# Optimization experiments

Hardware: AMD Instinct MI355X
Metric: run time of the kernel (lower is better)

## Reference

```python
import jax, jax.numpy as jnp
import numpy as np
from jax import lax

DIM = 48
HEADS = 8
B, H, W = 4, 256, 256
EPS = 1e-12  # torch F.normalize eps


def conv1x1(x, w):
    # x: [b,c,h,w], w: [out,c] (1x1 conv, no bias)
    return jnp.einsum('bchw,oc->bohw', x, w)


def dwconv3x3(x, w):
    # depthwise 3x3, padding 1; w: [C,1,3,3]
    return lax.conv_general_dilated(
        x, w, window_strides=(1, 1), padding=((1, 1), (1, 1)),
        dimension_numbers=('NCHW', 'OIHW', 'NCHW'),
        feature_group_count=x.shape[1])


def setup_inputs() -> dict:
    key = jax.random.key(0)
    ks = jax.random.split(key, 8)
    s = 0.05
    return {
        'fea_0': jax.random.normal(ks[0], (B, DIM, H, W), jnp.float32),
        'fea_1': jax.random.normal(ks[1], (B, DIM, H, W), jnp.float32),
        'qk_w': jax.random.normal(ks[2], (2 * DIM, DIM), jnp.float32) * s,
        'qk_dw_w': jax.random.normal(ks[3], (2 * DIM, 1, 3, 3), jnp.float32) * s,
        'v_w': jax.random.normal(ks[4], (DIM, DIM), jnp.float32) * s,
        'v_dw_w': jax.random.normal(ks[5], (DIM, 1, 3, 3), jnp.float32) * s,
        'proj_w': jax.random.normal(ks[6], (DIM, DIM), jnp.float32) * s,
        'temperature': jnp.ones((HEADS, 1, 1), jnp.float32),
    }


def reference(fea_0, fea_1, qk_w, qk_dw_w, v_w, v_dw_w, proj_w, temperature):
    b, c, h, w = fea_0.shape
    ch = c // HEADS  # channels per head
    qk = dwconv3x3(conv1x1(fea_0, qk_w), qk_dw_w)
    q, k = jnp.split(qk, 2, axis=1)
    v = dwconv3x3(conv1x1(fea_1, v_w), v_dw_w)
    # [b, head, c_per_head, h*w]
    q = q.reshape(b, HEADS, ch, h * w)
    k = k.reshape(b, HEADS, ch, h * w)
    v = v.reshape(b, HEADS, ch, h * w)
    q = q / jnp.maximum(jnp.linalg.norm(q, axis=-1, keepdims=True), EPS)
    k = k / jnp.maximum(jnp.linalg.norm(k, axis=-1, keepdims=True), EPS)
    attn = jnp.einsum('bhcn,bhdn->bhcd', q, k) * temperature[None]
    attn = jax.nn.softmax(attn, axis=-1)
    out = jnp.einsum('bhcd,bhdn->bhcn', attn, v)
    out = out.reshape(b, c, h, w)
    return conv1x1(out, proj_w)
```

## Files before the change

### kernel.cpp

```cpp
#include <hip/hip_runtime.h>
#include <cstddef>

#define IMG 256
#define HW 65536
#define NB 4
#define NHEADS 8
#define TW 32
#define TH 16
#define HAW 34
#define HAH 18
#define HP2 (HAW*HAH)
#define NTILE 128
#define XSP 24

typedef short bf16x8 __attribute__((ext_vector_type(8)));
typedef float f32x4 __attribute__((ext_vector_type(4)));
typedef float f32x16 __attribute__((ext_vector_type(16)));

__device__ __forceinline__ unsigned short f2bf(float f) {
    unsigned int x = __float_as_uint(f);
    unsigned int r = (x + 0x7fffu + ((x >> 16) & 1u)) >> 16;
    return (unsigned short)r;
}

__device__ __forceinline__ int xcd_map(int bid, int nwg) {
    const int q = nwg >> 3, r = nwg & 7;
    const int x = bid & 7, i = bid >> 3;
    return (x < r ? x * (q + 1) : r * (q + 1) + (x - r) * q) + i;
}

__global__ __launch_bounds__(256) void prep_qcw_kernel(
    const float* __restrict__ qk_w, const float* __restrict__ qk_dw,
    unsigned short* __restrict__ qcwb) {
    const int idx = blockIdx.x * 256 + threadIdx.x;
    const int e16 = idx & 15;
    const int slot = (idx >> 4) & 127;
    const int tk = idx >> 11;
    const int ks = tk % 3;
    const int head = slot >> 4, sub = slot & 15;
    float v = 0.f;
    if (sub < 12) {
        const int row = (sub < 6) ? (head * 6 + sub) : (48 + head * 6 + (sub - 6));
        v = qk_dw[row * 9 + tk / 3] * qk_w[row * 48 + ks * 16 + e16];
    }
    qcwb[idx] = f2bf(v);
}

__global__ __launch_bounds__(512, 2) void fused_qk_stats_kernel(
    const float* __restrict__ fea0, const unsigned short* __restrict__ qcwb,
    float* __restrict__ stats) {
    __shared__ __align__(16) unsigned short xs[HP2][XSP];
    __shared__ __align__(16) unsigned short sg[8][16][72];
    __shared__ float sacc[384];

    const int tid = threadIdx.x;
    const int b = blockIdx.y;
    const int tile = xcd_map(blockIdx.x, NTILE);
    const int tx = tile & 7, ty = tile >> 3;
    const float* fb = fea0 + (size_t)b * 48 * HW;

    for (int i = tid; i < 384; i += 512) sacc[i] = 0.f;

    const int wave = tid >> 6, lane = tid & 63;
    const int l31 = lane & 31, lhi = lane >> 5;
    const int p = wave >> 2, g = wave & 3;

    f32x16 C[2][4];
#pragma unroll
    for (int m = 0; m < 2; ++m)
#pragma unroll
        for (int nf = 0; nf < 4; ++nf)
#pragma unroll
            for (int r = 0; r < 16; ++r) C[m][nf][r] = 0.f;

#pragma unroll
    for (int ks = 0; ks < 3; ++ks) {
        __syncthreads();
        for (int hp = tid; hp < HP2; hp += 512) {
            const int hx = hp % HAW, hy = hp / HAW;
            const int gx = tx * TW + hx - 1, gy = ty * TH + hy - 1;
            const bool inb = ((unsigned)gx < (unsigned)IMG) && ((unsigned)gy < (unsigned)IMG);
            const int pix = inb ? (gy * IMG + gx) : 0;
            bf16x8 t0, t1;
#pragma unroll
            for (int c = 0; c < 8; ++c) {
                t0[c] = (short)f2bf(inb ? fb[(size_t)(ks * 16 + c) * HW + pix] : 0.f);
                t1[c] = (short)f2bf(inb ? fb[(size_t)(ks * 16 + 8 + c) * HW + pix] : 0.f);
            }
            *(bf16x8*)&xs[hp][0] = t0;
            *(bf16x8*)&xs[hp][8] = t1;
        }
        __syncthreads();

#pragma unroll
        for (int tap = 0; tap < 9; ++tap) {
            const int dy = tap / 3, dx = tap % 3;
            const bf16x8 a0 = *(const bf16x8*)&qcwb[(size_t)((tap * 3 + ks) * 128 + p * 64 + l31) * 16 + lhi * 8];
            const bf16x8 a1 = *(const bf16x8*)&qcwb[(size_t)((tap * 3 + ks) * 128 + p * 64 + 32 + l31) * 16 + lhi * 8];
#pragma unroll
            for (int nf = 0; nf < 4; ++nf) {
                const int hrow = (4 * g + nf + dy) * HAW + l31 + dx;
                const bf16x8 bb = *(const bf16x8*)&xs[hrow][lhi * 8];
                C[0][nf] = __builtin_amdgcn_mfma_f32_32x32x16_bf16(a0, bb, C[0][nf], 0, 0, 0);
                C[1][nf] = __builtin_amdgcn_mfma_f32_32x32x16_bf16(a1, bb, C[1][nf], 0, 0, 0);
            }
        }
    }

    const int fr = lane & 15, fg = lane >> 4;

#define DO_STATS(CA, CB, hbase)                                                   \
    {                                                                             \
        _Pragma("unroll")                                                         \
        for (int hh = 0; hh < 2; ++hh) {                                          \
            _Pragma("unroll")                                                     \
            for (int rq = 0; rq < 2; ++rq) {                                      \
                if (!(rq && lhi)) {                                               \
                    _Pragma("unroll")                                             \
                    for (int j = 0; j < 4; ++j) {                                 \
                        const int sub = j + 8 * rq + 4 * lhi;                     \
                        sg[wave][sub][l31] = f2bf(CA[hh * 8 + rq * 4 + j]);       \
                        sg[wave][sub][32 + l31] = f2bf(CB[hh * 8 + rq * 4 + j]);  \
                    }                                                             \
                }                                                                 \
            }                                                                     \
            asm volatile("s_waitcnt lgkmcnt(0)" ::: "memory");                    \
            __builtin_amdgcn_sched_barrier(0);                                    \
            const bf16x8 a0 = *(const bf16x8*)&sg[wave][fr][fg * 8];              \
            const bf16x8 a1 = *(const bf16x8*)&sg[wave][fr][32 + fg * 8];         \
            asm volatile("s_waitcnt lgkmcnt(0)" ::: "memory");                    \
            __builtin_amdgcn_sched_barrier(0);                                    \
            f32x4 c4 = {0.f, 0.f, 0.f, 0.f};                                      \
            c4 = __builtin_amdgcn_mfma_f32_16x16x32_bf16(a0, a0, c4, 0, 0, 0);    \
            c4 = __builtin_amdgcn_mfma_f32_16x16x32_bf16(a1, a1, c4, 0, 0, 0);    \
            const int h = (hbase) + hh;                                           \
            _Pragma("unroll")                                                     \
            for (int r = 0; r < 4; ++r) {                                         \
                const int crow = fg * 4 + r;                                      \
                const float vv = c4[r];                                           \
                if (crow < 6) {                                                   \
                    if (fr == crow) atomicAdd(&sacc[h * 6 + crow], vv);           \
                    else if (fr >= 6 && fr < 12)                                  \
                        atomicAdd(&sacc[96 + h * 36 + crow * 6 + (fr - 6)], vv);  \
                } else if (crow < 12 && fr == crow) {                             \
                    atomicAdd(&sacc[48 + h * 6 + (crow - 6)], vv);                \
                }                                                                 \
            }                                                                     \
        }                                                                         \
    }

#pragma unroll
    for (int m = 0; m < 2; ++m) {
        DO_STATS(C[m][0], C[m][1], p * 4 + m * 2)
        DO_STATS(C[m][2], C[m][3], p * 4 + m * 2)
    }
#undef DO_STATS

    __syncthreads();
    for (int i = tid; i < 384; i += 512) atomicAdd(&stats[b * 384 + i], sacc[i]);
}

__global__ __launch_bounds__(256) void softmax_w2_cw_kernel(
    const float* __restrict__ stats, const float* __restrict__ proj_w,
    const float* __restrict__ temperature, const float* __restrict__ v_w,
    const float* __restrict__ v_dw, unsigned short* __restrict__ cwb) {
    const int b = blockIdx.x;
    const int tid = threadIdx.x;
    __shared__ float attn[NHEADS * 36];
    __shared__ float W2s[48 * 48];
    const float* sb = stats + b * 384;

    if (tid < 48) {
        const int h = tid / 6, cc = tid % 6;
        float nq = fmaxf(sqrtf(sb[tid]), 1e-12f);
        const float tmp = temperature[h];
        float lo[6];
#pragma unroll
        for (int d = 0; d < 6; ++d) {
            const float nk = fmaxf(sqrtf(sb[48 + h * 6 + d]), 1e-12f);
            lo[d] = sb[96 + h * 36 + cc * 6 + d] / (nq * nk) * tmp;
        }
        float m = lo[0];
#pragma unroll
        for (int d = 1; d < 6; ++d) m = fmaxf(m, lo[d]);
        float s = 0.f;
#pragma unroll
        for (int d = 0; d < 6; ++d) { lo[d] = expf(lo[d] - m); s += lo[d]; }
        const float inv = 1.f / s;
#pragma unroll
        for (int d = 0; d < 6; ++d) attn[h * 36 + cc * 6 + d] = lo[d] * inv;
    }
    __syncthreads();

    for (int idx = tid; idx < 48 * 48; idx += 256) {
        const int c = idx / 48, dg = idx % 48;
        const int h = dg / 6, hd = dg % 6;
        float s = 0.f;
#pragma unroll
        for (int cc = 0; cc < 6; ++cc)
            s = fmaf(proj_w[c * 48 + h * 6 + cc], attn[h * 36 + cc * 6 + hd], s);
        W2s[idx] = s;
    }
    __syncthreads();

    unsigned short* cb = cwb + (size_t)b * 27648;
    for (int pp = 0; pp < 9; ++pp) {
        const int pair = pp * 256 + tid;
        const int c = pair / 48, e = pair % 48;
        float acc[9];
#pragma unroll
        for (int t = 0; t < 9; ++t) acc[t] = 0.f;
        for (int d = 0; d < 48; ++d) {
            const float wv = W2s[c * 48 + d] * v_w[d * 48 + e];
#pragma unroll
            for (int t = 0; t < 9; ++t)
                acc[t] = fmaf(wv, v_dw[d * 9 + t], acc[t]);
        }
#pragma unroll
        for (int t = 0; t < 9; ++t)
            cb[(size_t)((t * 3 + (e >> 4)) * 64 + c) * 16 + (e & 15)] = f2bf(acc[t]);
    }
    for (int i = tid; i < 6912; i += 256) {
        const int e16 = i & 15;
        const int cp = 48 + ((i >> 4) & 15);
        const int tk = i >> 8;
        cb[(size_t)(tk * 64 + cp) * 16 + e16] = 0;
    }
}

__global__ __launch_bounds__(512, 2) void conv3x3_out_kernel(
    const float* __restrict__ fea1, const unsigned short* __restrict__ cwb,
    float* __restrict__ out) {
    __shared__ __align__(16) unsigned short xs[HP2][XSP];

    const int tid = threadIdx.x;
    const int b = blockIdx.y;
    const int tile = xcd_map(blockIdx.x, NTILE);
    const int tx = tile & 7, ty = tile >> 3;
    const float* fb = fea1 + (size_t)b * 48 * HW;
    const unsigned short* cb = cwb + (size_t)b * 27648;

    const int wave = tid >> 6, lane = tid & 63;
    const int l31 = lane & 31, lhi = lane >> 5;
    const int m = wave & 1, g = wave >> 1;

    f32x16 C[4];
#pragma unroll
    for (int nf = 0; nf < 4; ++nf)
#pragma unroll
        for (int r = 0; r < 16; ++r) C[nf][r] = 0.f;

#pragma unroll
    for (int ks = 0; ks < 3; ++ks) {
        __syncthreads();
        for (int hp = tid; hp < HP2; hp += 512) {
            const int hx = hp % HAW, hy = hp / HAW;
            const int gx = tx * TW + hx - 1, gy = ty * TH + hy - 1;
            const bool inb = ((unsigned)gx < (unsigned)IMG) && ((unsigned)gy < (unsigned)IMG);
            const int pix = inb ? (gy * IMG + gx) : 0;
            bf16x8 t0, t1;
#pragma unroll
            for (int c = 0; c < 8; ++c) {
                t0[c] = (short)f2bf(inb ? fb[(size_t)(ks * 16 + c) * HW + pix] : 0.f);
                t1[c] = (short)f2bf(inb ? fb[(size_t)(ks * 16 + 8 + c) * HW + pix] : 0.f);
            }
            *(bf16x8*)&xs[hp][0] = t0;
            *(bf16x8*)&xs[hp][8] = t1;
        }
        __syncthreads();

#pragma unroll
        for (int tap = 0; tap < 9; ++tap) {
            const int dy = tap / 3, dx = tap % 3;
            const bf16x8 a = *(const bf16x8*)&cb[(size_t)((tap * 3 + ks) * 64 + m * 32 + l31) * 16 + lhi * 8];
#pragma unroll
            for (int nf = 0; nf < 4; ++nf) {
                const int hrow = (4 * g + nf + dy) * HAW + l31 + dx;
                const bf16x8 bb = *(const bf16x8*)&xs[hrow][lhi * 8];
                C[nf] = __builtin_amdgcn_mfma_f32_32x32x16_bf16(a, bb, C[nf], 0, 0, 0);
            }
        }
    }

    float* ob = out + (size_t)b * 48 * HW;
#pragma unroll
    for (int nf = 0; nf < 4; ++nf) {
        const int gpx = (ty * TH + 4 * g + nf) * IMG + tx * TW + l31;
#pragma unroll
        for (int r = 0; r < 16; ++r) {
            const int och = m * 32 + (r & 3) + 8 * (r >> 2) + 4 * lhi;
            if (m == 0 || r < 8) ob[(size_t)och * HW + gpx] = C[nf][r];
        }
    }
}

extern "C" void kernel_launch(void* const* d_in, const int* in_sizes, int n_in,
                              void* d_out, int out_size, void* d_ws, size_t ws_size,
                              hipStream_t stream) {
    const float* fea0 = (const float*)d_in[0];
    const float* fea1 = (const float*)d_in[1];
    const float* qk_w = (const float*)d_in[2];
    const float* qk_dw = (const float*)d_in[3];
    const float* v_w = (const float*)d_in[4];
    const float* v_dw = (const float*)d_in[5];
    const float* proj_w = (const float*)d_in[6];
    const float* temperature = (const float*)d_in[7];
    float* out = (float*)d_out;

    char* ws = (char*)d_ws;
    float* stats = (float*)ws;
    unsigned short* cwb = (unsigned short*)(ws + 8192);
    unsigned short* qcwb = (unsigned short*)(ws + 8192 + 221184);

    hipMemsetAsync(stats, 0, (size_t)NB * 384 * sizeof(float), stream);

    prep_qcw_kernel<<<216, 256, 0, stream>>>(qk_w, qk_dw, qcwb);
    fused_qk_stats_kernel<<<dim3(NTILE, NB), 512, 0, stream>>>(fea0, qcwb, stats);
    softmax_w2_cw_kernel<<<NB, 256, 0, stream>>>(stats, proj_w, temperature, v_w, v_dw, cwb);
    conv3x3_out_kernel<<<dim3(NTILE, NB), 512, 0, stream>>>(fea1, cwb, out);
}
```

Baseline: 121.9 us.

## Halve tile height and split qk stats blocks across output-channel halves

Shrinks spatial tiles from 32x16 to 32x8 and 512-thread blocks to 256 threads, doubling the tile count. The qk stats kernel also gives each block only one half of the 128 output channels, so its grid is four times larger and each wave holds a single accumulator set. The aim is more concurrent blocks per CU and lower register pressure for better latency hiding. In exchange, halo reloads and fp32-to-bf16 conversion of fea0 roughly double in the stats kernel and fea1 halo overhead grows in the output kernel. The stats kernel also issues more global atomics.

```diff
diff --git a/kernel.cpp b/kernel.cpp
--- a/kernel.cpp
+++ b/kernel.cpp
@@ -6,12 +6,12 @@
 #define NB 4
 #define NHEADS 8
 #define TW 32
-#define TH 16
+#define TH 8
 #define HAW 34
-#define HAH 18
+#define HAH 10
 #define HP2 (HAW*HAH)
-#define NTILE 128
-#define XSP 24
+#define NTILE 256
+#define XSP 28
 
 typedef short bf16x8 __attribute__((ext_vector_type(8)));
 typedef float f32x4 __attribute__((ext_vector_type(4)));
@@ -46,37 +46,36 @@
     qcwb[idx] = f2bf(v);
 }
 
-__global__ __launch_bounds__(512, 2) void fused_qk_stats_kernel(
+__global__ __launch_bounds__(256, 4) void fused_qk_stats_kernel(
     const float* __restrict__ fea0, const unsigned short* __restrict__ qcwb,
     float* __restrict__ stats) {
     __shared__ __align__(16) unsigned short xs[HP2][XSP];
-    __shared__ __align__(16) unsigned short sg[8][16][72];
+    __shared__ __align__(16) unsigned short sg[4][16][72];
     __shared__ float sacc[384];
 
     const int tid = threadIdx.x;
     const int b = blockIdx.y;
-    const int tile = xcd_map(blockIdx.x, NTILE);
+    const int mp = xcd_map(blockIdx.x, 2 * NTILE);
+    const int tile = mp >> 1, p = mp & 1;
     const int tx = tile & 7, ty = tile >> 3;
     const float* fb = fea0 + (size_t)b * 48 * HW;
 
-    for (int i = tid; i < 384; i += 512) sacc[i] = 0.f;
+    for (int i = tid; i < 384; i += 256) sacc[i] = 0.f;
 
     const int wave = tid >> 6, lane = tid & 63;
     const int l31 = lane & 31, lhi = lane >> 5;
-    const int p = wave >> 2, g = wave & 3;
-
-    f32x16 C[2][4];
-#pragma unroll
-    for (int m = 0; m < 2; ++m)
-#pragma unroll
-        for (int nf = 0; nf < 4; ++nf)
-#pragma unroll
-            for (int r = 0; r < 16; ++r) C[m][nf][r] = 0.f;
+    const int m = wave & 1, g = wave >> 1;
+
+    f32x16 C[4];
+#pragma unroll
+    for (int nf = 0; nf < 4; ++nf)
+#pragma unroll
+        for (int r = 0; r < 16; ++r) C[nf][r] = 0.f;
 
 #pragma unroll
     for (int ks = 0; ks < 3; ++ks) {
         __syncthreads();
-        for (int hp = tid; hp < HP2; hp += 512) {
+        for (int hp = tid; hp < HP2; hp += 256) {
             const int hx = hp % HAW, hy = hp / HAW;
             const int gx = tx * TW + hx - 1, gy = ty * TH + hy - 1;
             const bool inb = ((unsigned)gx < (unsigned)IMG) && ((unsigned)gy < (unsigned)IMG);
@@ -95,14 +94,12 @@
 #pragma unroll
         for (int tap = 0; tap < 9; ++tap) {
             const int dy = tap / 3, dx = tap % 3;
-            const bf16x8 a0 = *(const bf16x8*)&qcwb[(size_t)((tap * 3 + ks) * 128 + p * 64 + l31) * 16 + lhi * 8];
-            const bf16x8 a1 = *(const bf16x8*)&qcwb[(size_t)((tap * 3 + ks) * 128 + p * 64 + 32 + l31) * 16 + lhi * 8];
+            const bf16x8 a = *(const bf16x8*)&qcwb[(size_t)((tap * 3 + ks) * 128 + p * 64 + m * 32 + l31) * 16 + lhi * 8];
 #pragma unroll
             for (int nf = 0; nf < 4; ++nf) {
                 const int hrow = (4 * g + nf + dy) * HAW + l31 + dx;
                 const bf16x8 bb = *(const bf16x8*)&xs[hrow][lhi * 8];
-                C[0][nf] = __builtin_amdgcn_mfma_f32_32x32x16_bf16(a0, bb, C[0][nf], 0, 0, 0);
-                C[1][nf] = __builtin_amdgcn_mfma_f32_32x32x16_bf16(a1, bb, C[1][nf], 0, 0, 0);
+                C[nf] = __builtin_amdgcn_mfma_f32_32x32x16_bf16(a, bb, C[nf], 0, 0, 0);
             }
         }
     }
@@ -149,15 +146,18 @@
         }                                                                         \
     }
 
-#pragma unroll
-    for (int m = 0; m < 2; ++m) {
-        DO_STATS(C[m][0], C[m][1], p * 4 + m * 2)
-        DO_STATS(C[m][2], C[m][3], p * 4 + m * 2)
-    }
+    DO_STATS(C[0], C[1], p * 4 + m * 2)
+    DO_STATS(C[2], C[3], p * 4 + m * 2)
 #undef DO_STATS
 
     __syncthreads();
-    for (int i = tid; i < 384; i += 512) atomicAdd(&stats[b * 384 + i], sacc[i]);
+    for (int i = tid; i < 192; i += 256) {
+        int idx;
+        if (i < 24) idx = p * 24 + i;
+        else if (i < 48) idx = 48 + p * 24 + (i - 24);
+        else idx = 96 + p * 144 + (i - 48);
+        atomicAdd(&stats[b * 384 + idx], sacc[idx]);
+    }
 }
 
 __global__ __launch_bounds__(256) void softmax_w2_cw_kernel(
@@ -228,7 +228,7 @@
     }
 }
 
-__global__ __launch_bounds__(512, 2) void conv3x3_out_kernel(
+__global__ __launch_bounds__(256, 4) void conv3x3_out_kernel(
     const float* __restrict__ fea1, const unsigned short* __restrict__ cwb,
     float* __restrict__ out) {
     __shared__ __align__(16) unsigned short xs[HP2][XSP];
@@ -253,7 +253,7 @@
 #pragma unroll
     for (int ks = 0; ks < 3; ++ks) {
         __syncthreads();
-        for (int hp = tid; hp < HP2; hp += 512) {
+        for (int hp = tid; hp < HP2; hp += 256) {
             const int hx = hp % HAW, hy = hp / HAW;
             const int gx = tx * TW + hx - 1, gy = ty * TH + hy - 1;
             const bool inb = ((unsigned)gx < (unsigned)IMG) && ((unsigned)gy < (unsigned)IMG);
@@ -315,7 +315,7 @@
     hipMemsetAsync(stats, 0, (size_t)NB * 384 * sizeof(float), stream);
 
     prep_qcw_kernel<<<216, 256, 0, stream>>>(qk_w, qk_dw, qcwb);
-    fused_qk_stats_kernel<<<dim3(NTILE, NB), 512, 0, stream>>>(fea0, qcwb, stats);
+    fused_qk_stats_kernel<<<dim3(2 * NTILE, NB), 256, 0, stream>>>(fea0, qcwb, stats);
     softmax_w2_cw_kernel<<<NB, 256, 0, stream>>>(stats, proj_w, temperature, v_w, v_dw, cwb);
-    conv3x3_out_kernel<<<dim3(NTILE, NB), 512, 0, stream>>>(fea1, cwb, out);
-}
+    conv3x3_out_kernel<<<dim3(NTILE, NB), 256, 0, stream>>>(fea1, cwb, out);
+}
```

Result: no change. 119.6 us (-2.0%).
